# Optimization experiments

Hardware: AMD Instinct MI355X
Metric: run time of the kernel (lower is better)

Reference implementation:

```python
import jax, jax.numpy as jnp
import numpy as np

N = 50000      # nodes
E = 500000     # edges
D_IN = 512
D_H = 512
D_OUT = 256


def setup_inputs() -> dict:
    key = jax.random.key(0)
    ks = jax.random.split(key, 5)
    x = jax.random.normal(ks[0], (N, D_IN), dtype=jnp.float32)
    edge_index = jax.random.randint(ks[1], (2, E), 0, N, dtype=jnp.int32)
    W1 = jax.random.normal(ks[2], (D_IN, D_H), dtype=jnp.float32) / np.float32(np.sqrt(D_IN))
    b1 = jnp.zeros((D_H,), dtype=jnp.float32)
    W2 = jax.random.normal(ks[3], (D_H, D_OUT), dtype=jnp.float32) / np.float32(np.sqrt(D_H))
    b2 = jnp.zeros((D_OUT,), dtype=jnp.float32)
    return {"x": x, "edge_index": edge_index, "W1": W1, "b1": b1, "W2": W2, "b2": b2}


def _gcn_conv(x, src, dst, W, b, n):
    # PyG GCNConv: h = X W; add self-loops; symmetric norm D^-1/2 (A+I) D^-1/2; aggregate at dst; + bias
    h = x @ W
    loop = jnp.arange(n, dtype=src.dtype)
    src_sl = jnp.concatenate([src, loop])
    dst_sl = jnp.concatenate([dst, loop])
    deg = jax.ops.segment_sum(jnp.ones_like(src_sl, dtype=h.dtype), dst_sl, num_segments=n)
    dinv = jnp.where(deg > 0, jax.lax.rsqrt(deg), 0.0)
    norm = dinv[src_sl] * dinv[dst_sl]                     # [E+N]
    msg = h[src_sl] * norm[:, None]                        # [E+N, out]
    out = jax.ops.segment_sum(msg, dst_sl, num_segments=n) # [N, out]
    return out + b


def reference(x, edge_index, W1, b1, W2, b2):
    # Encoder.forward in eval mode (dropout = identity, bn='none' = identity), ELU activation after each conv.
    src, dst = edge_index[0], edge_index[1]
    h = _gcn_conv(x, src, dst, W1, b1, N)
    h = jax.nn.elu(h)
    h = _gcn_conv(h, src, dst, W2, b2, N)
    return jax.nn.elu(h)
```

## Files before the change

kernel.cpp:

```cpp
#include <hip/hip_runtime.h>
#include <math.h>

#define N_NODES 50000
#define N_EDGES 500000
#define D_IN 512
#define D_H  512
#define D_OUT 256
#define NB 196

typedef __attribute__((ext_vector_type(8))) short bf16x8;
typedef __attribute__((ext_vector_type(8))) unsigned short ushort8;
typedef __attribute__((ext_vector_type(4))) float f32x4;

__device__ __forceinline__ float b2f(unsigned short u) {
    union { unsigned int i; float f; } v; v.i = ((unsigned int)u) << 16; return v.f;
}
__device__ __forceinline__ unsigned short f2b(float f) {
    unsigned int x = __float_as_uint(f);
    unsigned int r = (x + 0x7fffu + ((x >> 16) & 1u)) >> 16;
    return (unsigned short)r;
}


__global__ void k_wt(const float* __restrict__ W, unsigned short* __restrict__ Wt,
                     int K, int N) {
    __shared__ float t[32][33];
    const int bk = blockIdx.x * 32, bn = blockIdx.y * 32;
    const int tx = threadIdx.x, ty = threadIdx.y;
    for (int i = ty; i < 32; i += 8) t[i][tx] = W[(size_t)(bk + i) * N + bn + tx];
    __syncthreads();
    for (int i = ty; i < 32; i += 8)
        Wt[(size_t)(bn + i) * K + bk + tx] = f2b(t[tx][i]);
}


__global__ __launch_bounds__(256) void k_zero(int* __restrict__ p, int n) {
    int i = blockIdx.x * 256 + threadIdx.x;
    if (i < n) p[i] = 0;
}

__global__ __launch_bounds__(256) void k_indeg(const int* __restrict__ dst,
                                               int* __restrict__ indeg) {
    int i = blockIdx.x * 256 + threadIdx.x;
    if (i < N_EDGES) atomicAdd(&indeg[dst[i]], 1);
}

__global__ __launch_bounds__(256) void k_partials(const int* __restrict__ indeg,
                                                  int* __restrict__ bsum) {
    __shared__ int wsum[4];
    const int tid = threadIdx.x, lane = tid & 63, w = tid >> 6;
    const int i = blockIdx.x * 256 + tid;
    int v = (i < N_NODES) ? indeg[i] : 0;
#pragma unroll
    for (int o = 32; o > 0; o >>= 1) v += __shfl_down(v, o, 64);
    if (lane == 0) wsum[w] = v;
    __syncthreads();
    if (tid == 0) bsum[blockIdx.x] = wsum[0] + wsum[1] + wsum[2] + wsum[3];
}

__global__ __launch_bounds__(256) void k_scanb(const int* __restrict__ bsum,
                                               int* __restrict__ boff) {
    __shared__ int wsum[4];
    const int tid = threadIdx.x, lane = tid & 63, w = tid >> 6;
    const int v = (tid < NB) ? bsum[tid] : 0;
    int s = v;
#pragma unroll
    for (int o = 1; o < 64; o <<= 1) {
        int t = __shfl_up(s, o, 64);
        if (lane >= o) s += t;
    }
    if (lane == 63) wsum[w] = s;
    __syncthreads();
    int add = 0;
    for (int k = 0; k < w; ++k) add += wsum[k];
    if (tid < NB) boff[tid] = add + s - v;
}

__global__ __launch_bounds__(256) void k_finalize(const int* __restrict__ indeg,
                                                  const int* __restrict__ boff,
                                                  int* __restrict__ row_start,
                                                  int* __restrict__ cursor,
                                                  float* __restrict__ dinv) {
    __shared__ int wsum[4];
    const int tid = threadIdx.x, lane = tid & 63, w = tid >> 6;
    const int i = blockIdx.x * 256 + tid;
    const int v = (i < N_NODES) ? indeg[i] : 0;
    int s = v;
#pragma unroll
    for (int o = 1; o < 64; o <<= 1) {
        int t = __shfl_up(s, o, 64);
        if (lane >= o) s += t;
    }
    if (lane == 63) wsum[w] = s;
    __syncthreads();
    int add = boff[blockIdx.x];
    for (int k = 0; k < w; ++k) add += wsum[k];
    if (i < N_NODES) {
        const int excl = add + s - v;
        row_start[i] = excl;
        cursor[i] = excl;
        dinv[i] = rsqrtf((float)(1 + v));
    }
    if (i == N_NODES) row_start[N_NODES] = N_EDGES;
}

__global__ __launch_bounds__(256) void k_bucket(const int* __restrict__ src,
                                                const int* __restrict__ dst,
                                                int* __restrict__ cursor,
                                                int* __restrict__ csr_src) {
    int e = blockIdx.x * 256 + threadIdx.x;
    if (e >= N_EDGES) return;
    int pos = atomicAdd(&cursor[dst[e]], 1);
    csr_src[pos] = src[e];
}


__device__ __forceinline__ void gload16(const void* g, void* l) {
    __builtin_amdgcn_global_load_lds(
        (const __attribute__((address_space(1))) unsigned int*)g,
        (__attribute__((address_space(3))) unsigned int*)l, 16, 0, 0);
}

__global__ __launch_bounds__(256) void k_gemm_bf16(const unsigned short* __restrict__ A,
                                                   const unsigned short* __restrict__ Bt,
                                                   unsigned short* __restrict__ C,
                                                   int M, int N, int K) {
    __shared__ __align__(16) short As[128 * 32];
    __shared__ __align__(16) short Bs[128 * 32];

    const int tid = threadIdx.x;
    const int w = tid >> 6;
    const int lane = tid & 63;
    const int wr = w >> 1, wc = w & 1;
    const int brow = blockIdx.y * 128;
    const int bcol = blockIdx.x * 128;
    const int lhi = lane >> 4;
    const int llo = lane & 15;

    f32x4 acc[4][4];
#pragma unroll
    for (int i = 0; i < 4; ++i)
#pragma unroll
        for (int j = 0; j < 4; ++j) acc[i][j] = (f32x4){0.f, 0.f, 0.f, 0.f};

    const int srow = lane >> 2;
    const int schunk = (lane & 3) * 8;

    for (int kt = 0; kt < K; kt += 32) {
        __syncthreads();
#pragma unroll
        for (int i = 0; i < 2; ++i) {
            const int rbase = w * 32 + i * 16;
            int gr = brow + rbase + srow;
            gr = gr < M ? gr : M - 1;
            gload16(A + (size_t)gr * K + kt + schunk, &As[rbase * 32]);
            const int gc = bcol + rbase + srow;
            gload16(Bt + (size_t)gc * K + kt + schunk, &Bs[rbase * 32]);
        }
        __syncthreads();

        bf16x8 af[4], bfr[4];
#pragma unroll
        for (int mi = 0; mi < 4; ++mi)
            af[mi] = *(const bf16x8*)&As[(wr * 64 + mi * 16 + llo) * 32 + lhi * 8];
#pragma unroll
        for (int ni = 0; ni < 4; ++ni)
            bfr[ni] = *(const bf16x8*)&Bs[(wc * 64 + ni * 16 + llo) * 32 + lhi * 8];
#pragma unroll
        for (int mi = 0; mi < 4; ++mi)
#pragma unroll
            for (int ni = 0; ni < 4; ++ni)
                acc[mi][ni] = __builtin_amdgcn_mfma_f32_16x16x32_bf16(
                    af[mi], bfr[ni], acc[mi][ni], 0, 0, 0);
    }

#pragma unroll
    for (int mi = 0; mi < 4; ++mi) {
        const int row0 = brow + wr * 64 + mi * 16 + lhi * 4;
#pragma unroll
        for (int ni = 0; ni < 4; ++ni) {
            const int col = bcol + wc * 64 + ni * 16 + llo;
            const f32x4 v = acc[mi][ni];
#pragma unroll
            for (int r = 0; r < 4; ++r) {
                const int row = row0 + r;
                if (row < M) C[(size_t)row * N + col] = f2b(v[r]);
            }
        }
    }
}

__global__ __launch_bounds__(256) void k_gemm_a32(const float* __restrict__ A,
                                                  const unsigned short* __restrict__ Bt,
                                                  unsigned short* __restrict__ C,
                                                  int M, int N, int K) {
    __shared__ __align__(16) short As[128 * 32];
    __shared__ __align__(16) short Bs[128 * 32];

    const int tid = threadIdx.x;
    const int w = tid >> 6;
    const int lane = tid & 63;
    const int wr = w >> 1, wc = w & 1;
    const int brow = blockIdx.y * 128;
    const int bcol = blockIdx.x * 128;
    const int lhi = lane >> 4;
    const int llo = lane & 15;

    f32x4 acc[4][4];
#pragma unroll
    for (int i = 0; i < 4; ++i)
#pragma unroll
        for (int j = 0; j < 4; ++j) acc[i][j] = (f32x4){0.f, 0.f, 0.f, 0.f};

    const int arow = tid >> 1;
    const int ahalf = (tid & 1) * 16;
    int gr = brow + arow;
    gr = gr < M ? gr : M - 1;
    const float* aptr = A + (size_t)gr * K + ahalf;

    const int srow = lane >> 2;
    const int schunk = (lane & 3) * 8;

    for (int kt = 0; kt < K; kt += 32) {
        const float4 a0 = *(const float4*)(aptr + kt);
        const float4 a1 = *(const float4*)(aptr + kt + 4);
        const float4 a2 = *(const float4*)(aptr + kt + 8);
        const float4 a3 = *(const float4*)(aptr + kt + 12);

        __syncthreads();
#pragma unroll
        for (int i = 0; i < 2; ++i) {
            const int rbase = w * 32 + i * 16;
            const int gc = bcol + rbase + srow;
            gload16(Bt + (size_t)gc * K + kt + schunk, &Bs[rbase * 32]);
        }
        ushort8 c0, c1;
        c0[0] = f2b(a0.x); c0[1] = f2b(a0.y); c0[2] = f2b(a0.z); c0[3] = f2b(a0.w);
        c0[4] = f2b(a1.x); c0[5] = f2b(a1.y); c0[6] = f2b(a1.z); c0[7] = f2b(a1.w);
        c1[0] = f2b(a2.x); c1[1] = f2b(a2.y); c1[2] = f2b(a2.z); c1[3] = f2b(a2.w);
        c1[4] = f2b(a3.x); c1[5] = f2b(a3.y); c1[6] = f2b(a3.z); c1[7] = f2b(a3.w);
        *(ushort8*)&As[arow * 32 + ahalf] = c0;
        *(ushort8*)&As[arow * 32 + ahalf + 8] = c1;
        __syncthreads();

        bf16x8 af[4], bfr[4];
#pragma unroll
        for (int mi = 0; mi < 4; ++mi)
            af[mi] = *(const bf16x8*)&As[(wr * 64 + mi * 16 + llo) * 32 + lhi * 8];
#pragma unroll
        for (int ni = 0; ni < 4; ++ni)
            bfr[ni] = *(const bf16x8*)&Bs[(wc * 64 + ni * 16 + llo) * 32 + lhi * 8];
#pragma unroll
        for (int mi = 0; mi < 4; ++mi)
#pragma unroll
            for (int ni = 0; ni < 4; ++ni)
                acc[mi][ni] = __builtin_amdgcn_mfma_f32_16x16x32_bf16(
                    af[mi], bfr[ni], acc[mi][ni], 0, 0, 0);
    }

#pragma unroll
    for (int mi = 0; mi < 4; ++mi) {
        const int row0 = brow + wr * 64 + mi * 16 + lhi * 4;
#pragma unroll
        for (int ni = 0; ni < 4; ++ni) {
            const int col = bcol + wc * 64 + ni * 16 + llo;
            const f32x4 v = acc[mi][ni];
#pragma unroll
            for (int r = 0; r < 4; ++r) {
                const int row = row0 + r;
                if (row < M) C[(size_t)row * N + col] = f2b(v[r]);
            }
        }
    }
}


template <int D, bool BF16_OUT>
__global__ __launch_bounds__(256) void k_aggregate(const unsigned short* __restrict__ H,
                                                   const float* __restrict__ bias,
                                                   void* __restrict__ outv,
                                                   const int* __restrict__ row_start,
                                                   const int* __restrict__ csr_src,
                                                   const float* __restrict__ dinv) {
    const int wid = threadIdx.x >> 6;
    const int lane = threadIdx.x & 63;
    int n, c0;
    if (D == 512) { n = blockIdx.x * 4 + wid; c0 = lane * 8; }
    else          { n = blockIdx.x * 8 + wid * 2 + (lane >> 5); c0 = (lane & 31) * 8; }
    if (n >= N_NODES) return;

    const float di = dinv[n];
    float acc[8];
    {
        const float ws = di * di;
        ushort8 v = *(const ushort8*)(H + (size_t)n * D + c0);
#pragma unroll
        for (int e = 0; e < 8; ++e) acc[e] = b2f(v[e]) * ws;
    }

    const int e0 = row_start[n];
    const int e1 = row_start[n + 1];
    int j = e0;
    for (; j + 8 <= e1; j += 8) {
        int s[8];
        float wgt[8];
#pragma unroll
        for (int q = 0; q < 8; ++q) s[q] = csr_src[j + q];
#pragma unroll
        for (int q = 0; q < 8; ++q) wgt[q] = dinv[s[q]] * di;
#pragma unroll
        for (int h = 0; h < 2; ++h) {
            const ushort8 v0 = *(const ushort8*)(H + (size_t)s[h * 4 + 0] * D + c0);
            const ushort8 v1 = *(const ushort8*)(H + (size_t)s[h * 4 + 1] * D + c0);
            const ushort8 v2 = *(const ushort8*)(H + (size_t)s[h * 4 + 2] * D + c0);
            const ushort8 v3 = *(const ushort8*)(H + (size_t)s[h * 4 + 3] * D + c0);
#pragma unroll
            for (int e = 0; e < 8; ++e) {
                acc[e] = fmaf(b2f(v0[e]), wgt[h * 4 + 0], acc[e]);
                acc[e] = fmaf(b2f(v1[e]), wgt[h * 4 + 1], acc[e]);
                acc[e] = fmaf(b2f(v2[e]), wgt[h * 4 + 2], acc[e]);
                acc[e] = fmaf(b2f(v3[e]), wgt[h * 4 + 3], acc[e]);
            }
        }
    }
    for (; j + 4 <= e1; j += 4) {
        const int s0 = csr_src[j + 0];
        const int s1 = csr_src[j + 1];
        const int s2 = csr_src[j + 2];
        const int s3 = csr_src[j + 3];
        const float w0 = dinv[s0] * di;
        const float w1 = dinv[s1] * di;
        const float w2 = dinv[s2] * di;
        const float w3 = dinv[s3] * di;
        const ushort8 v0 = *(const ushort8*)(H + (size_t)s0 * D + c0);
        const ushort8 v1 = *(const ushort8*)(H + (size_t)s1 * D + c0);
        const ushort8 v2 = *(const ushort8*)(H + (size_t)s2 * D + c0);
        const ushort8 v3 = *(const ushort8*)(H + (size_t)s3 * D + c0);
#pragma unroll
        for (int e = 0; e < 8; ++e) {
            acc[e] = fmaf(b2f(v0[e]), w0, acc[e]);
            acc[e] = fmaf(b2f(v1[e]), w1, acc[e]);
            acc[e] = fmaf(b2f(v2[e]), w2, acc[e]);
            acc[e] = fmaf(b2f(v3[e]), w3, acc[e]);
        }
    }
    for (; j < e1; ++j) {
        const int s = csr_src[j];
        const float ws = dinv[s] * di;
        const ushort8 v = *(const ushort8*)(H + (size_t)s * D + c0);
#pragma unroll
        for (int e = 0; e < 8; ++e) acc[e] = fmaf(b2f(v[e]), ws, acc[e]);
    }

#pragma unroll
    for (int e = 0; e < 8; ++e) {
        float t = acc[e] + bias[c0 + e];
        acc[e] = t > 0.f ? t : expf(t) - 1.f;
    }

    if (BF16_OUT) {
        ushort8 o;
#pragma unroll
        for (int e = 0; e < 8; ++e) o[e] = f2b(acc[e]);
        *(ushort8*)((unsigned short*)outv + (size_t)n * D + c0) = o;
    } else {
        float* orow = (float*)outv + (size_t)n * D + c0;
        *(float4*)orow = make_float4(acc[0], acc[1], acc[2], acc[3]);
        *(float4*)(orow + 4) = make_float4(acc[4], acc[5], acc[6], acc[7]);
    }
}


extern "C" void kernel_launch(void* const* d_in, const int* in_sizes, int n_in,
                              void* d_out, int out_size, void* d_ws, size_t ws_size,
                              hipStream_t stream) {
    const float* x  = (const float*)d_in[0];
    const int* ei   = (const int*)d_in[1];
    const int* src  = ei;
    const int* dst  = ei + N_EDGES;
    const float* W1 = (const float*)d_in[2];
    const float* b1 = (const float*)d_in[3];
    const float* W2 = (const float*)d_in[4];
    const float* b2 = (const float*)d_in[5];
    float* out = (float*)d_out;

    char* ws = (char*)d_ws;
    size_t off = 0;
    auto alloc = [&](size_t bytes) -> void* {
        void* p = ws + off;
        off = (off + bytes + 255) & ~(size_t)255;
        return p;
    };
    int*   indeg     = (int*)alloc((size_t)N_NODES * 4);
    int*   bsum      = (int*)alloc((size_t)NB * 4);
    int*   boff      = (int*)alloc((size_t)NB * 4);
    int*   row_start = (int*)alloc((size_t)(N_NODES + 1) * 4);
    int*   cursor    = (int*)alloc((size_t)N_NODES * 4);
    int*   csr_src   = (int*)alloc((size_t)N_EDGES * 4);
    float* dinv      = (float*)alloc((size_t)N_NODES * 4);
    unsigned short* W1t  = (unsigned short*)alloc((size_t)D_H * D_IN * 2);
    unsigned short* W2t  = (unsigned short*)alloc((size_t)D_OUT * D_H * 2);
    unsigned short* H1   = (unsigned short*)alloc((size_t)N_NODES * D_H * 2);
    unsigned short* out1 = (unsigned short*)alloc((size_t)N_NODES * D_H * 2);
    unsigned short* H2   = (unsigned short*)alloc((size_t)N_NODES * D_OUT * 2);

    k_zero<<<(N_NODES + 255) / 256, 256, 0, stream>>>(indeg, N_NODES);
    k_indeg<<<(N_EDGES + 255) / 256, 256, 0, stream>>>(dst, indeg);
    k_partials<<<NB, 256, 0, stream>>>(indeg, bsum);
    k_scanb<<<1, 256, 0, stream>>>(bsum, boff);
    k_finalize<<<NB, 256, 0, stream>>>(indeg, boff, row_start, cursor, dinv);
    k_bucket<<<(N_EDGES + 255) / 256, 256, 0, stream>>>(src, dst, cursor, csr_src);

    {
        dim3 b(32, 8);
        dim3 g1(D_IN / 32, D_H / 32);
        k_wt<<<g1, b, 0, stream>>>(W1, W1t, D_IN, D_H);
        dim3 g2(D_H / 32, D_OUT / 32);
        k_wt<<<g2, b, 0, stream>>>(W2, W2t, D_H, D_OUT);
    }

    dim3 gg1(D_H / 128, (N_NODES + 127) / 128);
    k_gemm_a32<<<gg1, 256, 0, stream>>>(x, W1t, H1, N_NODES, D_H, D_IN);
    k_aggregate<512, true><<<(N_NODES + 3) / 4, 256, 0, stream>>>(H1, b1, out1, row_start, csr_src, dinv);

    dim3 gg2(D_OUT / 128, (N_NODES + 127) / 128);
    k_gemm_bf16<<<gg2, 256, 0, stream>>>(out1, W2t, H2, N_NODES, D_OUT, D_H);
    k_aggregate<256, false><<<(N_NODES + 7) / 8, 256, 0, stream>>>(H2, b2, out, row_start, csr_src, dinv);
}
```

Before: 323.6 us.

## Double-buffer GEMM LDS tiles and remap blocks for XCD-aware locality

Both GEMM kernels now use two LDS buffers, so the next K-tile is prefetched (global-to-LDS for B and bf16 A; fp32 A held in registers and converted after the MFMAs) while the current tile is computed. This leaves one barrier per iteration instead of two. Blocks are launched on a 1D grid and remapped so the 8 XCDs each take contiguous row blocks, with all column blocks of a row group adjacent, to improve L2 reuse of A rows. The cost is twice the LDS per block, which may lower occupancy, plus some padded blocks that exit early.

```diff
diff --git a/kernel.cpp b/kernel.cpp
--- a/kernel.cpp
+++ b/kernel.cpp
@@ -124,16 +124,24 @@
 __global__ __launch_bounds__(256) void k_gemm_bf16(const unsigned short* __restrict__ A,
                                                    const unsigned short* __restrict__ Bt,
                                                    unsigned short* __restrict__ C,
-                                                   int M, int N, int K) {
-    __shared__ __align__(16) short As[128 * 32];
-    __shared__ __align__(16) short Bs[128 * 32];
+                                                   int M, int N, int K,
+                                                   int ncb, int nrb) {
+    __shared__ __align__(16) short As[2][128 * 32];
+    __shared__ __align__(16) short Bs[2][128 * 32];
+
+    const int bid = blockIdx.x;
+    const int xcd = bid & 7;
+    const int sidx = bid >> 3;
+    const int cb = sidx % ncb;
+    const int rb = (sidx / ncb) * 8 + xcd;
+    if (rb >= nrb) return;
+    const int brow = rb * 128;
+    const int bcol = cb * 128;
 
     const int tid = threadIdx.x;
     const int w = tid >> 6;
     const int lane = tid & 63;
     const int wr = w >> 1, wc = w & 1;
-    const int brow = blockIdx.y * 128;
-    const int bcol = blockIdx.x * 128;
     const int lhi = lane >> 4;
     const int llo = lane & 15;
 
@@ -146,32 +154,50 @@
     const int srow = lane >> 2;
     const int schunk = (lane & 3) * 8;
 
-    for (int kt = 0; kt < K; kt += 32) {
-        __syncthreads();
-#pragma unroll
-        for (int i = 0; i < 2; ++i) {
-            const int rbase = w * 32 + i * 16;
-            int gr = brow + rbase + srow;
-            gr = gr < M ? gr : M - 1;
-            gload16(A + (size_t)gr * K + kt + schunk, &As[rbase * 32]);
-            const int gc = bcol + rbase + srow;
-            gload16(Bt + (size_t)gc * K + kt + schunk, &Bs[rbase * 32]);
-        }
-        __syncthreads();
+    const int nt = K / 32;
+
+#pragma unroll
+    for (int i = 0; i < 2; ++i) {
+        const int rbase = w * 32 + i * 16;
+        int gr = brow + rbase + srow;
+        gr = gr < M ? gr : M - 1;
+        gload16(A + (size_t)gr * K + schunk, &As[0][rbase * 32]);
+        const int gc = bcol + rbase + srow;
+        gload16(Bt + (size_t)gc * K + schunk, &Bs[0][rbase * 32]);
+    }
+    __syncthreads();
+
+    int cur = 0;
+    for (int t = 0; t < nt; ++t) {
+        if (t + 1 < nt) {
+            const int ktn = (t + 1) * 32;
+#pragma unroll
+            for (int i = 0; i < 2; ++i) {
+                const int rbase = w * 32 + i * 16;
+                int gr = brow + rbase + srow;
+                gr = gr < M ? gr : M - 1;
+                gload16(A + (size_t)gr * K + ktn + schunk, &As[cur ^ 1][rbase * 32]);
+                const int gc = bcol + rbase + srow;
+                gload16(Bt + (size_t)gc * K + ktn + schunk, &Bs[cur ^ 1][rbase * 32]);
+            }
+        }
 
         bf16x8 af[4], bfr[4];
 #pragma unroll
         for (int mi = 0; mi < 4; ++mi)
-            af[mi] = *(const bf16x8*)&As[(wr * 64 + mi * 16 + llo) * 32 + lhi * 8];
+            af[mi] = *(const bf16x8*)&As[cur][(wr * 64 + mi * 16 + llo) * 32 + lhi * 8];
 #pragma unroll
         for (int ni = 0; ni < 4; ++ni)
-            bfr[ni] = *(const bf16x8*)&Bs[(wc * 64 + ni * 16 + llo) * 32 + lhi * 8];
+            bfr[ni] = *(const bf16x8*)&Bs[cur][(wc * 64 + ni * 16 + llo) * 32 + lhi * 8];
 #pragma unroll
         for (int mi = 0; mi < 4; ++mi)
 #pragma unroll
             for (int ni = 0; ni < 4; ++ni)
                 acc[mi][ni] = __builtin_amdgcn_mfma_f32_16x16x32_bf16(
                     af[mi], bfr[ni], acc[mi][ni], 0, 0, 0);
+
+        __syncthreads();
+        cur ^= 1;
     }
 
 #pragma unroll
@@ -193,16 +219,24 @@
 __global__ __launch_bounds__(256) void k_gemm_a32(const float* __restrict__ A,
                                                   const unsigned short* __restrict__ Bt,
                                                   unsigned short* __restrict__ C,
-                                                  int M, int N, int K) {
-    __shared__ __align__(16) short As[128 * 32];
-    __shared__ __align__(16) short Bs[128 * 32];
+                                                  int M, int N, int K,
+                                                  int ncb, int nrb) {
+    __shared__ __align__(16) short As[2][128 * 32];
+    __shared__ __align__(16) short Bs[2][128 * 32];
+
+    const int bid = blockIdx.x;
+    const int xcd = bid & 7;
+    const int sidx = bid >> 3;
+    const int cb = sidx % ncb;
+    const int rb = (sidx / ncb) * 8 + xcd;
+    if (rb >= nrb) return;
+    const int brow = rb * 128;
+    const int bcol = cb * 128;
 
     const int tid = threadIdx.x;
     const int w = tid >> 6;
     const int lane = tid & 63;
     const int wr = w >> 1, wc = w & 1;
-    const int brow = blockIdx.y * 128;
-    const int bcol = blockIdx.x * 128;
     const int lhi = lane >> 4;
     const int llo = lane & 15;
 
@@ -221,41 +255,73 @@
     const int srow = lane >> 2;
     const int schunk = (lane & 3) * 8;
 
-    for (int kt = 0; kt < K; kt += 32) {
-        const float4 a0 = *(const float4*)(aptr + kt);
-        const float4 a1 = *(const float4*)(aptr + kt + 4);
-        const float4 a2 = *(const float4*)(aptr + kt + 8);
-        const float4 a3 = *(const float4*)(aptr + kt + 12);
-
-        __syncthreads();
+    const int nt = K / 32;
+
+    {
+        const float4 a0 = *(const float4*)(aptr + 0);
+        const float4 a1 = *(const float4*)(aptr + 4);
+        const float4 a2 = *(const float4*)(aptr + 8);
+        const float4 a3 = *(const float4*)(aptr + 12);
 #pragma unroll
         for (int i = 0; i < 2; ++i) {
             const int rbase = w * 32 + i * 16;
             const int gc = bcol + rbase + srow;
-            gload16(Bt + (size_t)gc * K + kt + schunk, &Bs[rbase * 32]);
+            gload16(Bt + (size_t)gc * K + schunk, &Bs[0][rbase * 32]);
         }
         ushort8 c0, c1;
         c0[0] = f2b(a0.x); c0[1] = f2b(a0.y); c0[2] = f2b(a0.z); c0[3] = f2b(a0.w);
         c0[4] = f2b(a1.x); c0[5] = f2b(a1.y); c0[6] = f2b(a1.z); c0[7] = f2b(a1.w);
         c1[0] = f2b(a2.x); c1[1] = f2b(a2.y); c1[2] = f2b(a2.z); c1[3] = f2b(a2.w);
         c1[4] = f2b(a3.x); c1[5] = f2b(a3.y); c1[6] = f2b(a3.z); c1[7] = f2b(a3.w);
-        *(ushort8*)&As[arow * 32 + ahalf] = c0;
-        *(ushort8*)&As[arow * 32 + ahalf + 8] = c1;
-        __syncthreads();
+        *(ushort8*)&As[0][arow * 32 + ahalf] = c0;
+        *(ushort8*)&As[0][arow * 32 + ahalf + 8] = c1;
+    }
+    __syncthreads();
+
+    int cur = 0;
+    for (int t = 0; t < nt; ++t) {
+        float4 a0, a1, a2, a3;
+        const bool more = (t + 1 < nt);
+        if (more) {
+            const int ktn = (t + 1) * 32;
+            a0 = *(const float4*)(aptr + ktn);
+            a1 = *(const float4*)(aptr + ktn + 4);
+            a2 = *(const float4*)(aptr + ktn + 8);
+            a3 = *(const float4*)(aptr + ktn + 12);
+#pragma unroll
+            for (int i = 0; i < 2; ++i) {
+                const int rbase = w * 32 + i * 16;
+                const int gc = bcol + rbase + srow;
+                gload16(Bt + (size_t)gc * K + ktn + schunk, &Bs[cur ^ 1][rbase * 32]);
+            }
+        }
 
         bf16x8 af[4], bfr[4];
 #pragma unroll
         for (int mi = 0; mi < 4; ++mi)
-            af[mi] = *(const bf16x8*)&As[(wr * 64 + mi * 16 + llo) * 32 + lhi * 8];
+            af[mi] = *(const bf16x8*)&As[cur][(wr * 64 + mi * 16 + llo) * 32 + lhi * 8];
 #pragma unroll
         for (int ni = 0; ni < 4; ++ni)
-            bfr[ni] = *(const bf16x8*)&Bs[(wc * 64 + ni * 16 + llo) * 32 + lhi * 8];
+            bfr[ni] = *(const bf16x8*)&Bs[cur][(wc * 64 + ni * 16 + llo) * 32 + lhi * 8];
 #pragma unroll
         for (int mi = 0; mi < 4; ++mi)
 #pragma unroll
             for (int ni = 0; ni < 4; ++ni)
                 acc[mi][ni] = __builtin_amdgcn_mfma_f32_16x16x32_bf16(
                     af[mi], bfr[ni], acc[mi][ni], 0, 0, 0);
+
+        if (more) {
+            ushort8 c0, c1;
+            c0[0] = f2b(a0.x); c0[1] = f2b(a0.y); c0[2] = f2b(a0.z); c0[3] = f2b(a0.w);
+            c0[4] = f2b(a1.x); c0[5] = f2b(a1.y); c0[6] = f2b(a1.z); c0[7] = f2b(a1.w);
+            c1[0] = f2b(a2.x); c1[1] = f2b(a2.y); c1[2] = f2b(a2.z); c1[3] = f2b(a2.w);
+            c1[4] = f2b(a3.x); c1[5] = f2b(a3.y); c1[6] = f2b(a3.z); c1[7] = f2b(a3.w);
+            *(ushort8*)&As[cur ^ 1][arow * 32 + ahalf] = c0;
+            *(ushort8*)&As[cur ^ 1][arow * 32 + ahalf + 8] = c1;
+        }
+
+        __syncthreads();
+        cur ^= 1;
     }
 
 #pragma unroll
@@ -419,11 +485,20 @@
         k_wt<<<g2, b, 0, stream>>>(W2, W2t, D_H, D_OUT);
     }
 
-    dim3 gg1(D_H / 128, (N_NODES + 127) / 128);
-    k_gemm_a32<<<gg1, 256, 0, stream>>>(x, W1t, H1, N_NODES, D_H, D_IN);
+    const int nrb = (N_NODES + 127) / 128;
+    const int rgrp = (nrb + 7) / 8;
+
+    {
+        const int ncb = D_H / 128;
+        const int nblk = 8 * ncb * rgrp;
+        k_gemm_a32<<<nblk, 256, 0, stream>>>(x, W1t, H1, N_NODES, D_H, D_IN, ncb, nrb);
+    }
     k_aggregate<512, true><<<(N_NODES + 3) / 4, 256, 0, stream>>>(H1, b1, out1, row_start, csr_src, dinv);
 
-    dim3 gg2(D_OUT / 128, (N_NODES + 127) / 128);
-    k_gemm_bf16<<<gg2, 256, 0, stream>>>(out1, W2t, H2, N_NODES, D_OUT, D_H);
+    {
+        const int ncb = D_OUT / 128;
+        const int nblk = 8 * ncb * rgrp;
+        k_gemm_bf16<<<nblk, 256, 0, stream>>>(out1, W2t, H2, N_NODES, D_OUT, D_H, ncb, nrb);
+    }
     k_aggregate<256, false><<<(N_NODES + 7) / 8, 256, 0, stream>>>(H2, b2, out, row_start, csr_src, dinv);
 }
```

Result: faster. 313.8 us (-3.0%).

## Merge GEMMs into double-buffered 256x256 tile kernel with swizzled LDS

Applied to the files above, without the earlier changes.

Replaces the two 128x128 GEMM kernels with one templated 256x256-tile kernel using 512 threads. It double-buffers the LDS tiles so the next K-slice loads overlap the MFMA work, and XOR-swizzles the LDS chunk layout to cut bank conflicts. For the fp32 input, the bf16 conversion and LDS store are deferred until after the MFMAs. Larger tiles improve operand reuse but raise register and LDS pressure and leave fewer blocks to fill the CUs (the second GEMM has only 196 blocks).

```diff
diff --git a/kernel.cpp b/kernel.cpp
--- a/kernel.cpp
+++ b/kernel.cpp
@@ -121,62 +121,138 @@
         (__attribute__((address_space(3))) unsigned int*)l, 16, 0, 0);
 }
 
-__global__ __launch_bounds__(256) void k_gemm_bf16(const unsigned short* __restrict__ A,
-                                                   const unsigned short* __restrict__ Bt,
-                                                   unsigned short* __restrict__ C,
-                                                   int M, int N, int K) {
-    __shared__ __align__(16) short As[128 * 32];
-    __shared__ __align__(16) short Bs[128 * 32];
+template <bool A32>
+__global__ __launch_bounds__(512, 2) void k_gemm256(const void* __restrict__ Av,
+                                                    const unsigned short* __restrict__ Bt,
+                                                    unsigned short* __restrict__ C,
+                                                    int M, int N, int K) {
+    __shared__ __align__(16) short As[2][256 * 32];
+    __shared__ __align__(16) short Bs[2][256 * 32];
 
     const int tid = threadIdx.x;
-    const int w = tid >> 6;
+    const int wid = tid >> 6;
     const int lane = tid & 63;
-    const int wr = w >> 1, wc = w & 1;
-    const int brow = blockIdx.y * 128;
-    const int bcol = blockIdx.x * 128;
+    const int wr = wid >> 2;
+    const int wc = wid & 3;
+    const int brow = blockIdx.y * 256;
+    const int bcol = blockIdx.x * 256;
     const int lhi = lane >> 4;
     const int llo = lane & 15;
-
-    f32x4 acc[4][4];
-#pragma unroll
-    for (int i = 0; i < 4; ++i)
+    const int sw = (lhi ^ (llo & 3)) * 8;
+
+    f32x4 acc[8][4];
+#pragma unroll
+    for (int i = 0; i < 8; ++i)
 #pragma unroll
         for (int j = 0; j < 4; ++j) acc[i][j] = (f32x4){0.f, 0.f, 0.f, 0.f};
 
-    const int srow = lane >> 2;
-    const int schunk = (lane & 3) * 8;
-
-    for (int kt = 0; kt < K; kt += 32) {
-        __syncthreads();
-#pragma unroll
-        for (int i = 0; i < 2; ++i) {
-            const int rbase = w * 32 + i * 16;
-            int gr = brow + rbase + srow;
-            gr = gr < M ? gr : M - 1;
-            gload16(A + (size_t)gr * K + kt + schunk, &As[rbase * 32]);
-            const int gc = bcol + rbase + srow;
-            gload16(Bt + (size_t)gc * K + kt + schunk, &Bs[rbase * 32]);
+    const float* Af = (const float*)Av;
+    const unsigned short* Ab = (const unsigned short*)Av;
+
+    const int arow = tid >> 1;
+    const int ach0 = (tid & 1) * 2;
+    int gra = brow + arow;
+    gra = gra < M ? gra : M - 1;
+    const float* aptr32 = Af + (size_t)gra * K;
+    const int awch0 = (ach0 ^ (arow & 3)) * 8;
+    const int awch1 = ((ach0 + 1) ^ (arow & 3)) * 8;
+
+    const int nt = K / 32;
+
+#define STAGE_B(buf, kt)                                                          \
+    {                                                                             \
+        _Pragma("unroll")                                                         \
+        for (int g = 0; g < 2; ++g) {                                             \
+            const int cbase = g * 512 + wid * 64;                                 \
+            const int c = cbase + lane;                                           \
+            const int row = c >> 2;                                               \
+            const int sc = (c & 3) ^ (row & 3);                                   \
+            gload16(Bt + (size_t)(bcol + row) * K + (kt) * 32 + sc * 8,           \
+                    &Bs[buf][cbase * 8]);                                         \
+        }                                                                         \
+    }
+#define STAGE_A_BF16(buf, kt)                                                     \
+    {                                                                             \
+        _Pragma("unroll")                                                         \
+        for (int g = 0; g < 2; ++g) {                                             \
+            const int cbase = g * 512 + wid * 64;                                 \
+            const int c = cbase + lane;                                           \
+            int row = c >> 2;                                                     \
+            const int sc = (c & 3) ^ (row & 3);                                   \
+            int gr = brow + row;                                                  \
+            gr = gr < M ? gr : M - 1;                                             \
+            gload16(Ab + (size_t)gr * K + (kt) * 32 + sc * 8,                     \
+                    &As[buf][cbase * 8]);                                         \
+        }                                                                         \
+    }
+
+    if (A32) {
+        const float4 a0 = *(const float4*)(aptr32 + ach0 * 8);
+        const float4 a1 = *(const float4*)(aptr32 + ach0 * 8 + 4);
+        const float4 a2 = *(const float4*)(aptr32 + ach0 * 8 + 8);
+        const float4 a3 = *(const float4*)(aptr32 + ach0 * 8 + 12);
+        STAGE_B(0, 0);
+        ushort8 u0, u1;
+        u0[0] = f2b(a0.x); u0[1] = f2b(a0.y); u0[2] = f2b(a0.z); u0[3] = f2b(a0.w);
+        u0[4] = f2b(a1.x); u0[5] = f2b(a1.y); u0[6] = f2b(a1.z); u0[7] = f2b(a1.w);
+        u1[0] = f2b(a2.x); u1[1] = f2b(a2.y); u1[2] = f2b(a2.z); u1[3] = f2b(a2.w);
+        u1[4] = f2b(a3.x); u1[5] = f2b(a3.y); u1[6] = f2b(a3.z); u1[7] = f2b(a3.w);
+        *(ushort8*)&As[0][arow * 32 + awch0] = u0;
+        *(ushort8*)&As[0][arow * 32 + awch1] = u1;
+    } else {
+        STAGE_A_BF16(0, 0);
+        STAGE_B(0, 0);
+    }
+    __syncthreads();
+
+    int cur = 0;
+    for (int t = 0; t < nt; ++t) {
+        const bool more = (t + 1 < nt);
+        float4 a0, a1, a2, a3;
+        if (more) {
+            const int ktn = (t + 1) * 32;
+            if (A32) {
+                a0 = *(const float4*)(aptr32 + ktn + ach0 * 8);
+                a1 = *(const float4*)(aptr32 + ktn + ach0 * 8 + 4);
+                a2 = *(const float4*)(aptr32 + ktn + ach0 * 8 + 8);
+                a3 = *(const float4*)(aptr32 + ktn + ach0 * 8 + 12);
+            } else {
+                STAGE_A_BF16(cur ^ 1, t + 1);
+            }
+            STAGE_B(cur ^ 1, t + 1);
         }
-        __syncthreads();
-
-        bf16x8 af[4], bfr[4];
-#pragma unroll
-        for (int mi = 0; mi < 4; ++mi)
-            af[mi] = *(const bf16x8*)&As[(wr * 64 + mi * 16 + llo) * 32 + lhi * 8];
+
+        bf16x8 af[8], bf[4];
+#pragma unroll
+        for (int mi = 0; mi < 8; ++mi)
+            af[mi] = *(const bf16x8*)&As[cur][(wr * 128 + mi * 16 + llo) * 32 + sw];
 #pragma unroll
         for (int ni = 0; ni < 4; ++ni)
-            bfr[ni] = *(const bf16x8*)&Bs[(wc * 64 + ni * 16 + llo) * 32 + lhi * 8];
-#pragma unroll
-        for (int mi = 0; mi < 4; ++mi)
+            bf[ni] = *(const bf16x8*)&Bs[cur][(wc * 64 + ni * 16 + llo) * 32 + sw];
+#pragma unroll
+        for (int mi = 0; mi < 8; ++mi)
 #pragma unroll
             for (int ni = 0; ni < 4; ++ni)
                 acc[mi][ni] = __builtin_amdgcn_mfma_f32_16x16x32_bf16(
-                    af[mi], bfr[ni], acc[mi][ni], 0, 0, 0);
-    }
-
-#pragma unroll
-    for (int mi = 0; mi < 4; ++mi) {
-        const int row0 = brow + wr * 64 + mi * 16 + lhi * 4;
+                    af[mi], bf[ni], acc[mi][ni], 0, 0, 0);
+
+        if (A32 && more) {
+            ushort8 u0, u1;
+            u0[0] = f2b(a0.x); u0[1] = f2b(a0.y); u0[2] = f2b(a0.z); u0[3] = f2b(a0.w);
+            u0[4] = f2b(a1.x); u0[5] = f2b(a1.y); u0[6] = f2b(a1.z); u0[7] = f2b(a1.w);
+            u1[0] = f2b(a2.x); u1[1] = f2b(a2.y); u1[2] = f2b(a2.z); u1[3] = f2b(a2.w);
+            u1[4] = f2b(a3.x); u1[5] = f2b(a3.y); u1[6] = f2b(a3.z); u1[7] = f2b(a3.w);
+            *(ushort8*)&As[cur ^ 1][arow * 32 + awch0] = u0;
+            *(ushort8*)&As[cur ^ 1][arow * 32 + awch1] = u1;
+        }
+
+        __syncthreads();
+        cur ^= 1;
+    }
+
+#pragma unroll
+    for (int mi = 0; mi < 8; ++mi) {
+        const int row0 = brow + wr * 128 + mi * 16 + lhi * 4;
 #pragma unroll
         for (int ni = 0; ni < 4; ++ni) {
             const int col = bcol + wc * 64 + ni * 16 + llo;
@@ -188,90 +264,8 @@
             }
         }
     }
-}
-
-__global__ __launch_bounds__(256) void k_gemm_a32(const float* __restrict__ A,
-                                                  const unsigned short* __restrict__ Bt,
-                                                  unsigned short* __restrict__ C,
-                                                  int M, int N, int K) {
-    __shared__ __align__(16) short As[128 * 32];
-    __shared__ __align__(16) short Bs[128 * 32];
-
-    const int tid = threadIdx.x;
-    const int w = tid >> 6;
-    const int lane = tid & 63;
-    const int wr = w >> 1, wc = w & 1;
-    const int brow = blockIdx.y * 128;
-    const int bcol = blockIdx.x * 128;
-    const int lhi = lane >> 4;
-    const int llo = lane & 15;
-
-    f32x4 acc[4][4];
-#pragma unroll
-    for (int i = 0; i < 4; ++i)
-#pragma unroll
-        for (int j = 0; j < 4; ++j) acc[i][j] = (f32x4){0.f, 0.f, 0.f, 0.f};
-
-    const int arow = tid >> 1;
-    const int ahalf = (tid & 1) * 16;
-    int gr = brow + arow;
-    gr = gr < M ? gr : M - 1;
-    const float* aptr = A + (size_t)gr * K + ahalf;
-
-    const int srow = lane >> 2;
-    const int schunk = (lane & 3) * 8;
-
-    for (int kt = 0; kt < K; kt += 32) {
-        const float4 a0 = *(const float4*)(aptr + kt);
-        const float4 a1 = *(const float4*)(aptr + kt + 4);
-        const float4 a2 = *(const float4*)(aptr + kt + 8);
-        const float4 a3 = *(const float4*)(aptr + kt + 12);
-
-        __syncthreads();
-#pragma unroll
-        for (int i = 0; i < 2; ++i) {
-            const int rbase = w * 32 + i * 16;
-            const int gc = bcol + rbase + srow;
-            gload16(Bt + (size_t)gc * K + kt + schunk, &Bs[rbase * 32]);
-        }
-        ushort8 c0, c1;
-        c0[0] = f2b(a0.x); c0[1] = f2b(a0.y); c0[2] = f2b(a0.z); c0[3] = f2b(a0.w);
-        c0[4] = f2b(a1.x); c0[5] = f2b(a1.y); c0[6] = f2b(a1.z); c0[7] = f2b(a1.w);
-        c1[0] = f2b(a2.x); c1[1] = f2b(a2.y); c1[2] = f2b(a2.z); c1[3] = f2b(a2.w);
-        c1[4] = f2b(a3.x); c1[5] = f2b(a3.y); c1[6] = f2b(a3.z); c1[7] = f2b(a3.w);
-        *(ushort8*)&As[arow * 32 + ahalf] = c0;
-        *(ushort8*)&As[arow * 32 + ahalf + 8] = c1;
-        __syncthreads();
-
-        bf16x8 af[4], bfr[4];
-#pragma unroll
-        for (int mi = 0; mi < 4; ++mi)
-            af[mi] = *(const bf16x8*)&As[(wr * 64 + mi * 16 + llo) * 32 + lhi * 8];
-#pragma unroll
-        for (int ni = 0; ni < 4; ++ni)
-            bfr[ni] = *(const bf16x8*)&Bs[(wc * 64 + ni * 16 + llo) * 32 + lhi * 8];
-#pragma unroll
-        for (int mi = 0; mi < 4; ++mi)
-#pragma unroll
-            for (int ni = 0; ni < 4; ++ni)
-                acc[mi][ni] = __builtin_amdgcn_mfma_f32_16x16x32_bf16(
-                    af[mi], bfr[ni], acc[mi][ni], 0, 0, 0);
-    }
-
-#pragma unroll
-    for (int mi = 0; mi < 4; ++mi) {
-        const int row0 = brow + wr * 64 + mi * 16 + lhi * 4;
-#pragma unroll
-        for (int ni = 0; ni < 4; ++ni) {
-            const int col = bcol + wc * 64 + ni * 16 + llo;
-            const f32x4 v = acc[mi][ni];
-#pragma unroll
-            for (int r = 0; r < 4; ++r) {
-                const int row = row0 + r;
-                if (row < M) C[(size_t)row * N + col] = f2b(v[r]);
-            }
-        }
-    }
+#undef STAGE_B
+#undef STAGE_A_BF16
 }
 
 
@@ -419,11 +413,17 @@
         k_wt<<<g2, b, 0, stream>>>(W2, W2t, D_H, D_OUT);
     }
 
-    dim3 gg1(D_H / 128, (N_NODES + 127) / 128);
-    k_gemm_a32<<<gg1, 256, 0, stream>>>(x, W1t, H1, N_NODES, D_H, D_IN);
+    const int nmb = (N_NODES + 255) / 256;
+
+    {
+        dim3 g(D_H / 256, nmb);
+        k_gemm256<true><<<g, 512, 0, stream>>>(x, W1t, H1, N_NODES, D_H, D_IN);
+    }
     k_aggregate<512, true><<<(N_NODES + 3) / 4, 256, 0, stream>>>(H1, b1, out1, row_start, csr_src, dinv);
 
-    dim3 gg2(D_OUT / 128, (N_NODES + 127) / 128);
-    k_gemm_bf16<<<gg2, 256, 0, stream>>>(out1, W2t, H2, N_NODES, D_OUT, D_H);
+    {
+        dim3 g(D_OUT / 256, nmb);
+        k_gemm256<false><<<g, 512, 0, stream>>>(out1, W2t, H2, N_NODES, D_OUT, D_H);
+    }
     k_aggregate<256, false><<<(N_NODES + 7) / 8, 256, 0, stream>>>(H2, b2, out, row_start, csr_src, dinv);
 }
```

Measured after the change: 314.9 us. -2.7%, faster.
